# Kernel optimization log

Measured on AMD Instinct MI355X. Metric: run time of the kernel, lower is better.

Reference implementation:

```python
import jax, jax.numpy as jnp
import numpy as np

VOCAB, E, HID, HD, S, T = 50000, 1024, 1024, 512, 4096, 20
START, STOP, NEG = 18, 19, -10000.0


def setup_inputs() -> dict:
    key = jax.random.key(0)
    ks = jax.random.split(key, 16)
    scale = 0.05
    trans = jax.random.normal(ks[12], (T, T), jnp.float32)
    trans = trans.at[START, :].set(NEG).at[:, START].set(NEG)
    return {
        'sentence': jax.random.randint(ks[0], (S,), 0, VOCAB),
        'embed_table': jax.random.normal(ks[1], (VOCAB, E), jnp.float32) * scale,
        'w_ih_f': jax.random.normal(ks[2], (4 * HD, E), jnp.float32) * scale,
        'w_hh_f': jax.random.normal(ks[3], (4 * HD, HD), jnp.float32) * scale,
        'b_ih_f': jax.random.normal(ks[4], (4 * HD,), jnp.float32) * scale,
        'b_hh_f': jax.random.normal(ks[5], (4 * HD,), jnp.float32) * scale,
        'w_ih_b': jax.random.normal(ks[6], (4 * HD, E), jnp.float32) * scale,
        'w_hh_b': jax.random.normal(ks[7], (4 * HD, HD), jnp.float32) * scale,
        'b_ih_b': jax.random.normal(ks[8], (4 * HD,), jnp.float32) * scale,
        'b_hh_b': jax.random.normal(ks[9], (4 * HD,), jnp.float32) * scale,
        'w_out': jax.random.normal(ks[10], (T, HID), jnp.float32) * scale,
        'b_out': jax.random.normal(ks[11], (T,), jnp.float32) * scale,
        'transitions': trans,
        'h0': jax.random.normal(ks[13], (2, HD), jnp.float32),
        'c0': jax.random.normal(ks[14], (2, HD), jnp.float32),
    }


def _lstm_dir(pre, w_hh, b_hh, h0, c0, reverse):
    # pre: [S, 4HD] = x @ W_ih^T + b_ih (precomputed big GEMM)
    def step(carry, p):
        h, c = carry
        g = p + h @ w_hh.T + b_hh
        i, f, gg, o = jnp.split(g, 4, axis=-1)  # torch gate order i,f,g,o
        c = jax.nn.sigmoid(f) * c + jax.nn.sigmoid(i) * jnp.tanh(gg)
        h = jax.nn.sigmoid(o) * jnp.tanh(c)
        return (h, c), h
    _, hs = jax.lax.scan(step, (h0, c0), pre, reverse=reverse)
    return hs  # [S, HD], time-aligned in both directions


def _get_feats(sentence, embed_table, w_ih_f, w_hh_f, b_ih_f, b_hh_f,
               w_ih_b, w_hh_b, b_ih_b, b_hh_b, w_out, b_out, h0, c0):
    x = embed_table[sentence]                       # [S, E]
    hf = _lstm_dir(x @ w_ih_f.T + b_ih_f, w_hh_f, b_hh_f, h0[0], c0[0], False)
    hb = _lstm_dir(x @ w_ih_b.T + b_ih_b, w_hh_b, b_hh_b, h0[1], c0[1], True)
    lstm_out = jnp.concatenate([hf, hb], axis=-1)   # [S, HID]
    return lstm_out @ w_out.T + b_out               # [S, T]


def reference(sentence, embed_table, w_ih_f, w_hh_f, b_ih_f, b_hh_f,
              w_ih_b, w_hh_b, b_ih_b, b_hh_b, w_out, b_out,
              transitions, h0, c0):
    feats = _get_feats(sentence, embed_table, w_ih_f, w_hh_f, b_ih_f, b_hh_f,
                       w_ih_b, w_hh_b, b_ih_b, b_hh_b, w_out, b_out, h0, c0)
    # Viterbi decode
    init_v = jnp.full((T,), NEG, jnp.float32).at[START].set(0.0)

    def step(fv, feat):
        nt = fv[None, :] + transitions            # [T_cur, T_prev]
        best = jnp.argmax(nt, axis=1)             # backpointers [T]
        fv_new = jnp.max(nt, axis=1) + feat
        return fv_new, best

    fv_last, bptrs = jax.lax.scan(step, init_v, feats)
    terminal = fv_last + transitions[STOP]
    path_score = jnp.max(terminal)
    best_tag = jnp.argmax(terminal)

    def back(tag, bp):
        return bp[tag], tag
    _, path = jax.lax.scan(back, best_tag, bptrs, reverse=True)  # [S]
    return path_score, path
```

## Files before the change

### kernel.cpp

```cpp
#include <hip/hip_runtime.h>
#include <math.h>

#define S_LEN 4096
#define NTAG 20
#define TAG_STOP 19
#define NEGV -10000.0f


__global__ void init_ws(unsigned long long* hpub) {
    int i = blockIdx.x * 256 + threadIdx.x;
    if (i < 2048) hpub[i] = 0ull;
}

__device__ __forceinline__ float sigm(float x) { return 1.0f / (1.0f + expf(-x)); }

__launch_bounds__(256)
__global__ void pre_gemm(const int* __restrict__ sent, const float* __restrict__ embed,
                         const float* __restrict__ wf, const float* __restrict__ wb,
                         const float* __restrict__ bihf, const float* __restrict__ bhhf,
                         const float* __restrict__ bihb, const float* __restrict__ bhhb,
                         float* __restrict__ pre)
{
    __shared__ float As[16][68];
    __shared__ float Bs[16][136];
    __shared__ int   srow[64];
    const int tid = threadIdx.x;
    const int bm = blockIdx.x & 63;
    const int bn = blockIdx.x >> 6;
    const int pos0 = bm * 64, row0 = bn * 128;
    if (tid < 64) srow[tid] = sent[pos0 + tid];
    __syncthreads();

    const int tx = tid & 15, ty = tid >> 4;
    float acc[4][8];
    #pragma unroll
    for (int m = 0; m < 4; ++m)
        #pragma unroll
        for (int n = 0; n < 8; ++n) acc[m][n] = 0.f;

    for (int kt = 0; kt < 1024; kt += 16) {
        {
            int m = tid >> 2, kc = (tid & 3) * 4;
            const float* src = embed + (size_t)srow[m] * 1024 + kt + kc;
            float4 v = *(const float4*)src;
            As[kc+0][m] = v.x; As[kc+1][m] = v.y; As[kc+2][m] = v.z; As[kc+3][m] = v.w;
        }
        #pragma unroll
        for (int it = 0; it < 2; ++it) {
            int n = (tid >> 2) + it * 64;
            int kc = (tid & 3) * 4;
            int grow = row0 + n;
            const float* wsrc = (grow < 2048) ? (wf + (size_t)grow * 1024)
                                              : (wb + (size_t)(grow - 2048) * 1024);
            float4 v = *(const float4*)(wsrc + kt + kc);
            Bs[kc+0][n] = v.x; Bs[kc+1][n] = v.y; Bs[kc+2][n] = v.z; Bs[kc+3][n] = v.w;
        }
        __syncthreads();
        #pragma unroll
        for (int kk = 0; kk < 16; ++kk) {
            float a[4], b[8];
            float4 av = *(const float4*)&As[kk][ty * 4];
            a[0] = av.x; a[1] = av.y; a[2] = av.z; a[3] = av.w;
            float4 bv0 = *(const float4*)&Bs[kk][tx * 8];
            float4 bv1 = *(const float4*)&Bs[kk][tx * 8 + 4];
            b[0]=bv0.x; b[1]=bv0.y; b[2]=bv0.z; b[3]=bv0.w;
            b[4]=bv1.x; b[5]=bv1.y; b[6]=bv1.z; b[7]=bv1.w;
            #pragma unroll
            for (int m = 0; m < 4; ++m)
                #pragma unroll
                for (int n = 0; n < 8; ++n) acc[m][n] += a[m] * b[n];
        }
        __syncthreads();
    }
    #pragma unroll
    for (int m = 0; m < 4; ++m) {
        int pos = pos0 + ty * 4 + m;
        #pragma unroll
        for (int n = 0; n < 8; ++n) {
            int grow = row0 + tx * 8 + n;
            float bias = (grow < 2048) ? (bihf[grow] + bhhf[grow])
                                       : (bihb[grow - 2048] + bhhb[grow - 2048]);
            pre[(size_t)pos * 4096 + grow] = acc[m][n] + bias;
        }
    }
}

__device__ __forceinline__ unsigned long long agent_ld(const unsigned long long* p) {
    return __hip_atomic_load(p, __ATOMIC_RELAXED, __HIP_MEMORY_SCOPE_AGENT);
}

template<int P>
__device__ __forceinline__ void lstm_step(
    int s, int dir, int wg, int j, int ks, int su, bool own, int sidx, bool gate,
    const float* __restrict__ pre, const float* __restrict__ h0,
    float* __restrict__ hs, unsigned long long* pub,
    float (&buf)[2][576],
    const float (&wr0)[32], const float (&wr1)[32],
    const float (&wr2)[32], const float (&wr3)[32],
    float (&pf)[4], float& c_reg)
{
    if (s == 0) {
        buf[0][sidx] = h0[dir * 512 + su];
    } else if (!own) {
        const unsigned int expect = (unsigned int)s;
        const unsigned long long* p = &pub[P * 512 + su];
        unsigned long long u  = agent_ld(p);
        if ((unsigned int)(u >> 32) < expect) {
            unsigned long long u2 = agent_ld(p);
            while (true) {
                if ((unsigned int)(u >> 32) >= expect) break;
                u = agent_ld(p);
                if ((unsigned int)(u2 >> 32) >= expect) { u = u2; break; }
                u2 = agent_ld(p);
            }
        }
        buf[P][sidx] = __uint_as_float((unsigned int)u);
    }
    __syncthreads();

    float a0 = 0.f, a1 = 0.f, a2 = 0.f, a3 = 0.f;
    const float* hp = &buf[P][ks * 36];
    #pragma unroll
    for (int q = 0; q < 8; ++q) {
        float4 h4 = ((const float4*)hp)[q];
        a0 += wr0[q*4+0]*h4.x + wr0[q*4+1]*h4.y + wr0[q*4+2]*h4.z + wr0[q*4+3]*h4.w;
        a1 += wr1[q*4+0]*h4.x + wr1[q*4+1]*h4.y + wr1[q*4+2]*h4.z + wr1[q*4+3]*h4.w;
        a2 += wr2[q*4+0]*h4.x + wr2[q*4+1]*h4.y + wr2[q*4+2]*h4.z + wr2[q*4+3]*h4.w;
        a3 += wr3[q*4+0]*h4.x + wr3[q*4+1]*h4.y + wr3[q*4+2]*h4.z + wr3[q*4+3]*h4.w;
    }
    a0 += __shfl_xor(a0, 1); a0 += __shfl_xor(a0, 2); a0 += __shfl_xor(a0, 4); a0 += __shfl_xor(a0, 8);
    a1 += __shfl_xor(a1, 1); a1 += __shfl_xor(a1, 2); a1 += __shfl_xor(a1, 4); a1 += __shfl_xor(a1, 8);
    a2 += __shfl_xor(a2, 1); a2 += __shfl_xor(a2, 2); a2 += __shfl_xor(a2, 4); a2 += __shfl_xor(a2, 8);
    a3 += __shfl_xor(a3, 1); a3 += __shfl_xor(a3, 2); a3 += __shfl_xor(a3, 4); a3 += __shfl_xor(a3, 8);

    if (gate) {
        float gi = a0 + pf[0], gf = a1 + pf[1], gg = a2 + pf[2], go = a3 + pf[3];
        float cn = sigm(gf) * c_reg + sigm(gi) * tanhf(gg);
        float hN = sigm(go) * tanhf(cn);
        c_reg = cn;
        unsigned long long uv = ((unsigned long long)(unsigned int)(s + 1) << 32)
                              | (unsigned long long)__float_as_uint(hN);
        __hip_atomic_store(&pub[(P ^ 1) * 512 + j], uv,
                           __ATOMIC_RELAXED, __HIP_MEMORY_SCOPE_AGENT);
        const int pos = dir ? (S_LEN - 1 - s) : s;
        hs[((size_t)dir * S_LEN + pos) * 512 + j] = hN;
        buf[P ^ 1][j + 4 * wg] = hN;
        if (s + 2 < S_LEN) {
            const int pp = dir ? (S_LEN - 3 - s) : (s + 2);
            const float* pb = pre + (size_t)pp * 4096 + dir * 2048 + j;
            pf[0] = pb[0]; pf[1] = pb[512]; pf[2] = pb[1024]; pf[3] = pb[1536];
        }
    }
}

__launch_bounds__(512, 2)
__global__ void lstm_kernel(const float* __restrict__ pre,
                            const float* __restrict__ w_hh_f, const float* __restrict__ w_hh_b,
                            const float* __restrict__ h0, const float* __restrict__ c0,
                            float* __restrict__ hs, unsigned long long* __restrict__ h_pub)
{
    const int dir  = blockIdx.x >> 4;
    const int wg   = blockIdx.x & 15;
    const int tid  = threadIdx.x;
    const int wv   = tid >> 6;
    const int lane = tid & 63;
    const int rg   = lane >> 4;
    const int ks   = lane & 15;
    const int j    = wg * 32 + wv * 4 + rg;
    const float* w_hh = dir ? w_hh_b : w_hh_f;

    __shared__ float buf[2][576];

    float wr0[32], wr1[32], wr2[32], wr3[32];
    {
        const float* wbase = w_hh + (size_t)j * 512 + ks * 32;
        #pragma unroll
        for (int q = 0; q < 8; ++q) {
            float4 v0 = *(const float4*)(wbase + 0 * 262144 + q * 4);
            wr0[q*4+0] = v0.x; wr0[q*4+1] = v0.y; wr0[q*4+2] = v0.z; wr0[q*4+3] = v0.w;
            float4 v1 = *(const float4*)(wbase + 1 * 262144 + q * 4);
            wr1[q*4+0] = v1.x; wr1[q*4+1] = v1.y; wr1[q*4+2] = v1.z; wr1[q*4+3] = v1.w;
            float4 v2 = *(const float4*)(wbase + 2 * 262144 + q * 4);
            wr2[q*4+0] = v2.x; wr2[q*4+1] = v2.y; wr2[q*4+2] = v2.z; wr2[q*4+3] = v2.w;
            float4 v3 = *(const float4*)(wbase + 3 * 262144 + q * 4);
            wr3[q*4+0] = v3.x; wr3[q*4+1] = v3.y; wr3[q*4+2] = v3.z; wr3[q*4+3] = v3.w;
        }
    }

    const bool gate = (ks == 0);
    float c_reg = 0.f;
    float pfA[4] = {0,0,0,0}, pfB[4] = {0,0,0,0};
    if (gate) {
        c_reg = c0[dir * 512 + j];
        const int p0 = dir ? (S_LEN - 1) : 0;
        const int p1 = dir ? (S_LEN - 2) : 1;
        const float* b0 = pre + (size_t)p0 * 4096 + dir * 2048 + j;
        const float* b1 = pre + (size_t)p1 * 4096 + dir * 2048 + j;
        pfA[0] = b0[0]; pfA[1] = b0[512]; pfA[2] = b0[1024]; pfA[3] = b0[1536];
        pfB[0] = b1[0]; pfB[1] = b1[512]; pfB[2] = b1[1024]; pfB[3] = b1[1536];
    }

    const int  su   = tid;
    const bool own  = ((su >> 5) == wg);
    const int  sidx = su + ((su >> 5) << 2);
    unsigned long long* pub = h_pub + dir * 1024;

    for (int s = 0; s < S_LEN; s += 2) {
        lstm_step<0>(s,     dir, wg, j, ks, su, own, sidx, gate,
                     pre, h0, hs, pub, buf, wr0, wr1, wr2, wr3, pfA, c_reg);
        lstm_step<1>(s + 1, dir, wg, j, ks, su, own, sidx, gate,
                     pre, h0, hs, pub, buf, wr0, wr1, wr2, wr3, pfB, c_reg);
    }
}

__launch_bounds__(256)
__global__ void feats_kernel(const float* __restrict__ hs, const float* __restrict__ w_out,
                             const float* __restrict__ b_out, float* __restrict__ feats)
{
    const int pos = blockIdx.x;
    const int tid = threadIdx.x;
    __shared__ float hbuf[1024];
    __shared__ float red[160];
    {
        const float* hf = hs + (size_t)pos * 512;
        const float* hb = hs + ((size_t)S_LEN + pos) * 512;
        if (tid < 128) *(float4*)&hbuf[tid * 4]           = *(const float4*)&hf[tid * 4];
        else           *(float4*)&hbuf[512 + (tid-128)*4] = *(const float4*)&hb[(tid - 128) * 4];
    }
    __syncthreads();
    if (tid < 160) {
        int tag = tid >> 3, part = tid & 7;
        const float* wrow = w_out + (size_t)tag * 1024 + part * 128;
        const float* hrow = hbuf + part * 128;
        float sum = 0.f;
        #pragma unroll
        for (int q = 0; q < 32; ++q) {
            float4 a = ((const float4*)hrow)[q];
            float4 b = ((const float4*)wrow)[q];
            sum += a.x*b.x + a.y*b.y + a.z*b.z + a.w*b.w;
        }
        red[tid] = sum;
    }
    __syncthreads();
    if (tid < NTAG) {
        float sum = b_out[tid];
        #pragma unroll
        for (int pq = 0; pq < 8; ++pq) sum += red[tid * 8 + pq];
        feats[(size_t)pos * NTAG + tid] = sum;
    }
}

__launch_bounds__(256)
__global__ void viterbi_kernel(const float* __restrict__ feats, const float* __restrict__ trans,
                               unsigned char* __restrict__ bptr, float* __restrict__ out)
{
    __shared__ float feat_lds[64 * NTAG];
    __shared__ int sh_best;
    __shared__ unsigned char Mmap[8][NTAG];
    __shared__ unsigned char entry_s[8];
    const int tid = threadIdx.x;

    if (tid < 64) {
        const int lane = tid;
        const int i = (lane < NTAG) ? lane : (NTAG - 1);
        float trow[NTAG];
        #pragma unroll
        for (int jj = 0; jj < NTAG; ++jj) trow[jj] = trans[i * NTAG + jj];
        float fv[NTAG];
        #pragma unroll
        for (int jj = 0; jj < NTAG; ++jj) fv[jj] = (jj == 18) ? 0.f : NEGV;

        for (int blk = 0; blk < 64; ++blk) {
            #pragma unroll
            for (int q = 0; q < 20; ++q)
                feat_lds[q * 64 + lane] = feats[blk * 1280 + q * 64 + lane];
            for (int ss = 0; ss < 64; ++ss) {
                int s = blk * 64 + ss;
                float best = fv[0] + trow[0];
                int bj = 0;
                #pragma unroll
                for (int jj = 1; jj < NTAG; ++jj) {
                    float cand = fv[jj] + trow[jj];
                    if (cand > best) { best = cand; bj = jj; }
                }
                float fnew = best + feat_lds[ss * NTAG + i];
                if (lane < NTAG) bptr[s * NTAG + lane] = (unsigned char)bj;
                #pragma unroll
                for (int jj = 0; jj < NTAG; ++jj) fv[jj] = __shfl(fnew, jj);
            }
        }
        if (lane == 0) {
            float best = -1e30f; int bt = 0;
            for (int jj = 0; jj < NTAG; ++jj) {
                float t2 = fv[jj] + trans[TAG_STOP * NTAG + jj];
                if (t2 > best) { best = t2; bt = jj; }
            }
            out[0] = best;
            sh_best = bt;
        }
    }
    __syncthreads();
    if (tid < 160) {
        int c = tid / NTAG, e = tid % NTAG;
        int tag = e;
        for (int t = (c + 1) * 512 - 1; t >= c * 512; --t) tag = bptr[t * NTAG + tag];
        Mmap[c][e] = (unsigned char)tag;
    }
    __syncthreads();
    if (tid == 0) {
        int e = sh_best;
        entry_s[7] = (unsigned char)e;
        for (int c = 7; c >= 1; --c) { e = Mmap[c][e]; entry_s[c - 1] = (unsigned char)e; }
    }
    __syncthreads();
    if (tid < 8) {
        int c = tid;
        int tag = entry_s[c];
        out[1 + (c + 1) * 512 - 1] = (float)tag;
        for (int t = (c + 1) * 512 - 1; t > c * 512; --t) {
            tag = bptr[t * NTAG + tag];
            out[1 + t - 1] = (float)tag;
        }
    }
}

extern "C" void kernel_launch(void* const* d_in, const int* in_sizes, int n_in,
                              void* d_out, int out_size, void* d_ws, size_t ws_size,
                              hipStream_t stream) {
    (void)in_sizes; (void)n_in; (void)out_size; (void)ws_size;
    const int*   sent  = (const int*)d_in[0];
    const float* embed = (const float*)d_in[1];
    const float* wihf  = (const float*)d_in[2];
    const float* whhf  = (const float*)d_in[3];
    const float* bihf  = (const float*)d_in[4];
    const float* bhhf  = (const float*)d_in[5];
    const float* wihb  = (const float*)d_in[6];
    const float* whhb  = (const float*)d_in[7];
    const float* bihb  = (const float*)d_in[8];
    const float* bihb2 = (const float*)d_in[9];
    const float* wout  = (const float*)d_in[10];
    const float* bout  = (const float*)d_in[11];
    const float* trans = (const float*)d_in[12];
    const float* h0    = (const float*)d_in[13];
    const float* c0    = (const float*)d_in[14];
    const float* bhhb  = bihb2;

    char* ws = (char*)d_ws;
    unsigned long long* h_pub = (unsigned long long*)(ws + 4096);
    float* pre   = (float*)(ws + 65536);
    float* hs    = (float*)(ws + 65536 + (size_t)4096 * 4096 * 4);
    float* feats = (float*)(ws + 65536 + (size_t)4096 * 4096 * 4 + (size_t)2 * 4096 * 512 * 4);
    unsigned char* bptr = (unsigned char*)(feats + (size_t)S_LEN * NTAG);
    float* out = (float*)d_out;

    hipLaunchKernelGGL(init_ws, dim3(8), dim3(256), 0, stream, h_pub);
    hipLaunchKernelGGL(pre_gemm, dim3(2048), dim3(256), 0, stream,
                       sent, embed, wihf, wihb, bihf, bhhf, bihb, bhhb, pre);
    hipLaunchKernelGGL(lstm_kernel, dim3(32), dim3(512), 0, stream,
                       pre, whhf, whhb, h0, c0, hs, h_pub);
    hipLaunchKernelGGL(feats_kernel, dim3(S_LEN), dim3(256), 0, stream,
                       hs, wout, bout, feats);
    hipLaunchKernelGGL(viterbi_kernel, dim3(1), dim3(256), 0, stream,
                       feats, trans, bptr, out);
}
```

Baseline: 11.25 ms.

## Fuse input-projection GEMM into LSTM kernel with per-tile ready flags

Merges the pre-activation GEMM and the recurrent LSTM into one launch. Blocks 0-31 run the sequential recurrence while the remaining 2048 blocks compute GEMM tiles, ordered so both sequence ends finish first, and bump a per-row-tile ready counter that the LSTM blocks wait on before prefetching. This overlaps the GEMM with the long serial LSTM instead of running it beforehand. It risks GEMM blocks competing with the latency-critical LSTM blocks for CU resources, and it relies on the 32 LSTM blocks being resident. It also simplifies the spin loop and moves the publish store after the local writes.

```diff
diff --git a/kernel.cpp b/kernel.cpp
--- a/kernel.cpp
+++ b/kernel.cpp
@@ -7,86 +7,24 @@
 #define NEGV -10000.0f
 
 
-__global__ void init_ws(unsigned long long* hpub) {
+__global__ void init_ws(unsigned int* ready, unsigned long long* hpub) {
     int i = blockIdx.x * 256 + threadIdx.x;
+    if (i < 64) ready[i] = 0u;
     if (i < 2048) hpub[i] = 0ull;
 }
 
 __device__ __forceinline__ float sigm(float x) { return 1.0f / (1.0f + expf(-x)); }
-
-__launch_bounds__(256)
-__global__ void pre_gemm(const int* __restrict__ sent, const float* __restrict__ embed,
-                         const float* __restrict__ wf, const float* __restrict__ wb,
-                         const float* __restrict__ bihf, const float* __restrict__ bhhf,
-                         const float* __restrict__ bihb, const float* __restrict__ bhhb,
-                         float* __restrict__ pre)
-{
-    __shared__ float As[16][68];
-    __shared__ float Bs[16][136];
-    __shared__ int   srow[64];
-    const int tid = threadIdx.x;
-    const int bm = blockIdx.x & 63;
-    const int bn = blockIdx.x >> 6;
-    const int pos0 = bm * 64, row0 = bn * 128;
-    if (tid < 64) srow[tid] = sent[pos0 + tid];
-    __syncthreads();
-
-    const int tx = tid & 15, ty = tid >> 4;
-    float acc[4][8];
-    #pragma unroll
-    for (int m = 0; m < 4; ++m)
-        #pragma unroll
-        for (int n = 0; n < 8; ++n) acc[m][n] = 0.f;
-
-    for (int kt = 0; kt < 1024; kt += 16) {
-        {
-            int m = tid >> 2, kc = (tid & 3) * 4;
-            const float* src = embed + (size_t)srow[m] * 1024 + kt + kc;
-            float4 v = *(const float4*)src;
-            As[kc+0][m] = v.x; As[kc+1][m] = v.y; As[kc+2][m] = v.z; As[kc+3][m] = v.w;
-        }
-        #pragma unroll
-        for (int it = 0; it < 2; ++it) {
-            int n = (tid >> 2) + it * 64;
-            int kc = (tid & 3) * 4;
-            int grow = row0 + n;
-            const float* wsrc = (grow < 2048) ? (wf + (size_t)grow * 1024)
-                                              : (wb + (size_t)(grow - 2048) * 1024);
-            float4 v = *(const float4*)(wsrc + kt + kc);
-            Bs[kc+0][n] = v.x; Bs[kc+1][n] = v.y; Bs[kc+2][n] = v.z; Bs[kc+3][n] = v.w;
-        }
-        __syncthreads();
-        #pragma unroll
-        for (int kk = 0; kk < 16; ++kk) {
-            float a[4], b[8];
-            float4 av = *(const float4*)&As[kk][ty * 4];
-            a[0] = av.x; a[1] = av.y; a[2] = av.z; a[3] = av.w;
-            float4 bv0 = *(const float4*)&Bs[kk][tx * 8];
-            float4 bv1 = *(const float4*)&Bs[kk][tx * 8 + 4];
-            b[0]=bv0.x; b[1]=bv0.y; b[2]=bv0.z; b[3]=bv0.w;
-            b[4]=bv1.x; b[5]=bv1.y; b[6]=bv1.z; b[7]=bv1.w;
-            #pragma unroll
-            for (int m = 0; m < 4; ++m)
-                #pragma unroll
-                for (int n = 0; n < 8; ++n) acc[m][n] += a[m] * b[n];
-        }
-        __syncthreads();
-    }
-    #pragma unroll
-    for (int m = 0; m < 4; ++m) {
-        int pos = pos0 + ty * 4 + m;
-        #pragma unroll
-        for (int n = 0; n < 8; ++n) {
-            int grow = row0 + tx * 8 + n;
-            float bias = (grow < 2048) ? (bihf[grow] + bhhf[grow])
-                                       : (bihb[grow - 2048] + bhhb[grow - 2048]);
-            pre[(size_t)pos * 4096 + grow] = acc[m][n] + bias;
-        }
-    }
-}
 
 __device__ __forceinline__ unsigned long long agent_ld(const unsigned long long* p) {
     return __hip_atomic_load(p, __ATOMIC_RELAXED, __HIP_MEMORY_SCOPE_AGENT);
+}
+
+__device__ __forceinline__ void tile_wait(const unsigned int* ready, unsigned int& rdy_tile, int t) {
+    if ((unsigned int)t != rdy_tile) {
+        while (__hip_atomic_load(&ready[t], __ATOMIC_ACQUIRE, __HIP_MEMORY_SCOPE_AGENT) < 32u)
+            __builtin_amdgcn_s_sleep(4);
+        rdy_tile = (unsigned int)t;
+    }
 }
 
 template<int P>
@@ -94,6 +32,7 @@
     int s, int dir, int wg, int j, int ks, int su, bool own, int sidx, bool gate,
     const float* __restrict__ pre, const float* __restrict__ h0,
     float* __restrict__ hs, unsigned long long* pub,
+    const unsigned int* __restrict__ ready, unsigned int& rdy_tile,
     float (&buf)[2][576],
     const float (&wr0)[32], const float (&wr1)[32],
     const float (&wr2)[32], const float (&wr3)[32],
@@ -104,16 +43,8 @@
     } else if (!own) {
         const unsigned int expect = (unsigned int)s;
         const unsigned long long* p = &pub[P * 512 + su];
-        unsigned long long u  = agent_ld(p);
-        if ((unsigned int)(u >> 32) < expect) {
-            unsigned long long u2 = agent_ld(p);
-            while (true) {
-                if ((unsigned int)(u >> 32) >= expect) break;
-                u = agent_ld(p);
-                if ((unsigned int)(u2 >> 32) >= expect) { u = u2; break; }
-                u2 = agent_ld(p);
-            }
-        }
+        unsigned long long u = agent_ld(p);
+        while ((unsigned int)(u >> 32) < expect) u = agent_ld(p);
         buf[P][sidx] = __uint_as_float((unsigned int)u);
     }
     __syncthreads();
@@ -138,15 +69,16 @@
         float cn = sigm(gf) * c_reg + sigm(gi) * tanhf(gg);
         float hN = sigm(go) * tanhf(cn);
         c_reg = cn;
+        const int pos = dir ? (S_LEN - 1 - s) : s;
+        hs[((size_t)dir * S_LEN + pos) * 512 + j] = hN;
+        buf[P ^ 1][j + 4 * wg] = hN;
         unsigned long long uv = ((unsigned long long)(unsigned int)(s + 1) << 32)
                               | (unsigned long long)__float_as_uint(hN);
         __hip_atomic_store(&pub[(P ^ 1) * 512 + j], uv,
                            __ATOMIC_RELAXED, __HIP_MEMORY_SCOPE_AGENT);
-        const int pos = dir ? (S_LEN - 1 - s) : s;
-        hs[((size_t)dir * S_LEN + pos) * 512 + j] = hN;
-        buf[P ^ 1][j + 4 * wg] = hN;
         if (s + 2 < S_LEN) {
             const int pp = dir ? (S_LEN - 3 - s) : (s + 2);
+            tile_wait(ready, rdy_tile, pp >> 6);
             const float* pb = pre + (size_t)pp * 4096 + dir * 2048 + j;
             pf[0] = pb[0]; pf[1] = pb[512]; pf[2] = pb[1024]; pf[3] = pb[1536];
         }
@@ -154,14 +86,86 @@
 }
 
 __launch_bounds__(512, 2)
-__global__ void lstm_kernel(const float* __restrict__ pre,
-                            const float* __restrict__ w_hh_f, const float* __restrict__ w_hh_b,
-                            const float* __restrict__ h0, const float* __restrict__ c0,
-                            float* __restrict__ hs, unsigned long long* __restrict__ h_pub)
+__global__ void fused_kernel(const int* __restrict__ sent, const float* __restrict__ embed,
+                             const float* __restrict__ wf, const float* __restrict__ wb,
+                             const float* __restrict__ bihf, const float* __restrict__ bhhf,
+                             const float* __restrict__ bihb, const float* __restrict__ bhhb,
+                             float* __restrict__ pre,
+                             const float* __restrict__ w_hh_f, const float* __restrict__ w_hh_b,
+                             const float* __restrict__ h0, const float* __restrict__ c0,
+                             float* __restrict__ hs, unsigned long long* __restrict__ h_pub,
+                             unsigned int* __restrict__ ready)
 {
+    __shared__ float As[16][68];
+    __shared__ float Bs[16][136];
+    __shared__ int   srow[64];
+    __shared__ float buf[2][576];
+    const int tid = threadIdx.x;
+
+    if (blockIdx.x >= 32) {
+        const int gq = blockIdx.x - 32;
+        const int q  = gq >> 5;
+        const int bn = gq & 31;
+        const int bm = (q & 1) ? (63 - (q >> 1)) : (q >> 1);
+        const int pos0 = bm * 64, row0 = bn * 128;
+        if (tid < 64) srow[tid] = sent[pos0 + tid];
+        __syncthreads();
+
+        const int ty = tid >> 5, tx = tid & 31;
+        float acc[4][4];
+        #pragma unroll
+        for (int m = 0; m < 4; ++m)
+            #pragma unroll
+            for (int n = 0; n < 4; ++n) acc[m][n] = 0.f;
+
+        for (int kt = 0; kt < 1024; kt += 16) {
+            if (tid < 256) {
+                int m = tid >> 2, kc = (tid & 3) * 4;
+                float4 v = *(const float4*)(embed + (size_t)srow[m] * 1024 + kt + kc);
+                As[kc+0][m] = v.x; As[kc+1][m] = v.y; As[kc+2][m] = v.z; As[kc+3][m] = v.w;
+            }
+            {
+                int n = tid >> 2, kc = (tid & 3) * 4;
+                int grow = row0 + n;
+                const float* wsrc = (grow < 2048) ? (wf + (size_t)grow * 1024)
+                                                  : (wb + (size_t)(grow - 2048) * 1024);
+                float4 v = *(const float4*)(wsrc + kt + kc);
+                Bs[kc+0][n] = v.x; Bs[kc+1][n] = v.y; Bs[kc+2][n] = v.z; Bs[kc+3][n] = v.w;
+            }
+            __syncthreads();
+            #pragma unroll
+            for (int kk = 0; kk < 16; ++kk) {
+                float4 av = *(const float4*)&As[kk][ty * 4];
+                float4 bv = *(const float4*)&Bs[kk][tx * 4];
+                float a[4] = {av.x, av.y, av.z, av.w};
+                float b[4] = {bv.x, bv.y, bv.z, bv.w};
+                #pragma unroll
+                for (int m = 0; m < 4; ++m)
+                    #pragma unroll
+                    for (int n = 0; n < 4; ++n) acc[m][n] += a[m] * b[n];
+            }
+            __syncthreads();
+        }
+        #pragma unroll
+        for (int m = 0; m < 4; ++m) {
+            int pos = pos0 + ty * 4 + m;
+            #pragma unroll
+            for (int n = 0; n < 4; ++n) {
+                int grow = row0 + tx * 4 + n;
+                float bias = (grow < 2048) ? (bihf[grow] + bhhf[grow])
+                                           : (bihb[grow - 2048] + bhhb[grow - 2048]);
+                __hip_atomic_store(&pre[(size_t)pos * 4096 + grow], acc[m][n] + bias,
+                                   __ATOMIC_RELAXED, __HIP_MEMORY_SCOPE_AGENT);
+            }
+        }
+        __syncthreads();
+        if (tid == 0)
+            __hip_atomic_fetch_add(&ready[bm], 1u, __ATOMIC_RELEASE, __HIP_MEMORY_SCOPE_AGENT);
+        return;
+    }
+
     const int dir  = blockIdx.x >> 4;
     const int wg   = blockIdx.x & 15;
-    const int tid  = threadIdx.x;
     const int wv   = tid >> 6;
     const int lane = tid & 63;
     const int rg   = lane >> 4;
@@ -169,31 +173,32 @@
     const int j    = wg * 32 + wv * 4 + rg;
     const float* w_hh = dir ? w_hh_b : w_hh_f;
 
-    __shared__ float buf[2][576];
-
     float wr0[32], wr1[32], wr2[32], wr3[32];
     {
         const float* wbase = w_hh + (size_t)j * 512 + ks * 32;
         #pragma unroll
-        for (int q = 0; q < 8; ++q) {
-            float4 v0 = *(const float4*)(wbase + 0 * 262144 + q * 4);
-            wr0[q*4+0] = v0.x; wr0[q*4+1] = v0.y; wr0[q*4+2] = v0.z; wr0[q*4+3] = v0.w;
-            float4 v1 = *(const float4*)(wbase + 1 * 262144 + q * 4);
-            wr1[q*4+0] = v1.x; wr1[q*4+1] = v1.y; wr1[q*4+2] = v1.z; wr1[q*4+3] = v1.w;
-            float4 v2 = *(const float4*)(wbase + 2 * 262144 + q * 4);
-            wr2[q*4+0] = v2.x; wr2[q*4+1] = v2.y; wr2[q*4+2] = v2.z; wr2[q*4+3] = v2.w;
-            float4 v3 = *(const float4*)(wbase + 3 * 262144 + q * 4);
-            wr3[q*4+0] = v3.x; wr3[q*4+1] = v3.y; wr3[q*4+2] = v3.z; wr3[q*4+3] = v3.w;
+        for (int qq = 0; qq < 8; ++qq) {
+            float4 v0 = *(const float4*)(wbase + 0 * 262144 + qq * 4);
+            wr0[qq*4+0] = v0.x; wr0[qq*4+1] = v0.y; wr0[qq*4+2] = v0.z; wr0[qq*4+3] = v0.w;
+            float4 v1 = *(const float4*)(wbase + 1 * 262144 + qq * 4);
+            wr1[qq*4+0] = v1.x; wr1[qq*4+1] = v1.y; wr1[qq*4+2] = v1.z; wr1[qq*4+3] = v1.w;
+            float4 v2 = *(const float4*)(wbase + 2 * 262144 + qq * 4);
+            wr2[qq*4+0] = v2.x; wr2[qq*4+1] = v2.y; wr2[qq*4+2] = v2.z; wr2[qq*4+3] = v2.w;
+            float4 v3 = *(const float4*)(wbase + 3 * 262144 + qq * 4);
+            wr3[qq*4+0] = v3.x; wr3[qq*4+1] = v3.y; wr3[qq*4+2] = v3.z; wr3[qq*4+3] = v3.w;
         }
     }
 
     const bool gate = (ks == 0);
+    unsigned int rdy_tile = 0xffffffffu;
     float c_reg = 0.f;
     float pfA[4] = {0,0,0,0}, pfB[4] = {0,0,0,0};
     if (gate) {
         c_reg = c0[dir * 512 + j];
         const int p0 = dir ? (S_LEN - 1) : 0;
         const int p1 = dir ? (S_LEN - 2) : 1;
+        tile_wait(ready, rdy_tile, p0 >> 6);
+        tile_wait(ready, rdy_tile, p1 >> 6);
         const float* b0 = pre + (size_t)p0 * 4096 + dir * 2048 + j;
         const float* b1 = pre + (size_t)p1 * 4096 + dir * 2048 + j;
         pfA[0] = b0[0]; pfA[1] = b0[512]; pfA[2] = b0[1024]; pfA[3] = b0[1536];
@@ -207,9 +212,9 @@
 
     for (int s = 0; s < S_LEN; s += 2) {
         lstm_step<0>(s,     dir, wg, j, ks, su, own, sidx, gate,
-                     pre, h0, hs, pub, buf, wr0, wr1, wr2, wr3, pfA, c_reg);
+                     pre, h0, hs, pub, ready, rdy_tile, buf, wr0, wr1, wr2, wr3, pfA, c_reg);
         lstm_step<1>(s + 1, dir, wg, j, ks, su, own, sidx, gate,
-                     pre, h0, hs, pub, buf, wr0, wr1, wr2, wr3, pfB, c_reg);
+                     pre, h0, hs, pub, ready, rdy_tile, buf, wr0, wr1, wr2, wr3, pfB, c_reg);
     }
 }
 
@@ -337,15 +342,15 @@
     const float* wihb  = (const float*)d_in[6];
     const float* whhb  = (const float*)d_in[7];
     const float* bihb  = (const float*)d_in[8];
-    const float* bihb2 = (const float*)d_in[9];
+    const float* bhhb  = (const float*)d_in[9];
     const float* wout  = (const float*)d_in[10];
     const float* bout  = (const float*)d_in[11];
     const float* trans = (const float*)d_in[12];
     const float* h0    = (const float*)d_in[13];
     const float* c0    = (const float*)d_in[14];
-    const float* bhhb  = bihb2;
 
     char* ws = (char*)d_ws;
+    unsigned int* ready       = (unsigned int*)ws;
     unsigned long long* h_pub = (unsigned long long*)(ws + 4096);
     float* pre   = (float*)(ws + 65536);
     float* hs    = (float*)(ws + 65536 + (size_t)4096 * 4096 * 4);
@@ -353,11 +358,10 @@
     unsigned char* bptr = (unsigned char*)(feats + (size_t)S_LEN * NTAG);
     float* out = (float*)d_out;
 
-    hipLaunchKernelGGL(init_ws, dim3(8), dim3(256), 0, stream, h_pub);
-    hipLaunchKernelGGL(pre_gemm, dim3(2048), dim3(256), 0, stream,
-                       sent, embed, wihf, wihb, bihf, bhhf, bihb, bhhb, pre);
-    hipLaunchKernelGGL(lstm_kernel, dim3(32), dim3(512), 0, stream,
-                       pre, whhf, whhb, h0, c0, hs, h_pub);
+    hipLaunchKernelGGL(init_ws, dim3(8), dim3(256), 0, stream, ready, h_pub);
+    hipLaunchKernelGGL(fused_kernel, dim3(32 + 2048), dim3(512), 0, stream,
+                       sent, embed, wihf, wihb, bihf, bhhf, bihb, bhhb, pre,
+                       whhf, whhb, h0, c0, hs, h_pub, ready);
     hipLaunchKernelGGL(feats_kernel, dim3(S_LEN), dim3(256), 0, stream,
                        hs, wout, bout, feats);
     hipLaunchKernelGGL(viterbi_kernel, dim3(1), dim3(256), 0, stream,
```

New measurement: 10.35 ms. -8.0%, faster.
